# Kernel tuning notes

Hardware: AMD Instinct MI355X
Metric: run time of the kernel (lower is better)

Reference implementation:

```python
import jax, jax.numpy as jnp
import numpy as np

N_EMBD = 256
B, T = 2, 512


def setup_inputs() -> dict:
    key = jax.random.key(0)
    kx, ks, kv = jax.random.split(key, 3)
    x = jax.random.normal(kx, (B, T, N_EMBD), dtype=jnp.float32)
    # init std 0.02 per nn.init.normal_(..., std=0.02); keeps I - scaled well-conditioned
    skew_param = 0.02 * jax.random.normal(ks, (N_EMBD, N_EMBD), dtype=jnp.float32)
    vector = 0.02 * jax.random.normal(kv, (1, N_EMBD), dtype=jnp.float32)
    return {"x": x, "skew_param": skew_param, "vector": vector}


def reference(x, skew_param, vector):
    n = skew_param.shape[0]
    skew = skew_param - skew_param.T                      # (n, n), skew-symmetric
    # scaled[b,t,i,j] = x[b,t,i] * skew[i,j]  -> (B, T, n, n)
    scaled = x[..., :, None] * skew
    eye = jnp.eye(n, dtype=x.dtype)
    # Cayley transform: (I - scaled)^{-1} (I + scaled), batched over (B, T)
    q = jnp.linalg.solve(eye - scaled, eye + scaled)      # (B, T, n, n)
    # (1, n) @ (B, T, n, n) -> (B, T, n) after squeezing the row dim
    out = jnp.einsum('n,btnm->btm', vector[0], q)
    return out
```

## Files before the change

### kernel.cpp

```cpp
#include <hip/hip_runtime.h>
#include <math.h>

#define N 256
#define G 4
#define BLK 1024
#define S1 10
#define S2 8
#define SP1 11
#define VS 268
#define UTS 280
#define RIDGE 3e-5f

typedef _Float16 half8v __attribute__((ext_vector_type(8)));
typedef float float4v __attribute__((ext_vector_type(4)));

#define OFF_K     0
#define OFF_UT0   47168
#define OFF_UT1   49408
#define OFF_ZTW   51648
#define OFF_GRAM  55744
#define OFF_L     57680
#define OFF_D     59280
#define ARENA_SZ  59456

#define LD_FRAG(base, t) (*(const half8v*)((base) + (mn & 3) * UTS + 32 * (t) + 8 * mq))

#define MATVEC(basep, dst) do {                                                        \
    float4v acc0 = {0.f, 0.f, 0.f, 0.f};                                               \
    float4v acc1 = {0.f, 0.f, 0.f, 0.f};                                               \
    _Pragma("unroll")                                                                  \
    for (int t = 0; t < 4; ++t) {                                                      \
        acc0 = __builtin_amdgcn_mfma_f32_16x16x32_f16(Shi[t], LD_FRAG(basep, t), acc0, 0, 0, 0);          \
        acc1 = __builtin_amdgcn_mfma_f32_16x16x32_f16(Shi[t + 4], LD_FRAG(basep, t + 4), acc1, 0, 0, 0);  \
    }                                                                                  \
    float4v accs = acc0 + acc1;                                                        \
    if (mn < 4) *(float4v*)(zTw + wv * 64 + mn * 16 + mq * 4) = accs;                  \
    dst = zTw[wv * 64 + g * 16 + coff];                                                \
} while (0)

__global__ __launch_bounds__(BLK, 4) void cayley_v12(const float* __restrict__ x_all,
                                                     const float* __restrict__ P,
                                                     const float* __restrict__ v_in,
                                                     float* __restrict__ out, int batch) {
    __shared__ __align__(16) char arena[ARENA_SZ];
    float* sK      = (float*)(arena + OFF_K);
    _Float16* uT0  = (_Float16*)(arena + OFF_UT0);
    _Float16* uT1  = (_Float16*)(arena + OFF_UT1);
    float* zTw     = (float*)(arena + OFF_ZTW);
    float* sGram   = (float*)(arena + OFF_GRAM);
    float* sL      = (float*)(arena + OFF_L);
    float* sD      = (float*)(arena + OFF_D);

    const int tid = threadIdx.x;
    const int lane = tid & 63, wv = tid >> 6;
    const int mn = lane & 15, mq = lane >> 4;
    const int c = tid >> 2, g = tid & 3;
    const int coff = lane >> 2;
    const int sys = blockIdx.x * G + g;
    const bool alive = sys < batch;

    half8v Shi[8];
    {
        const int r = 16 * wv + mn;
#pragma unroll
        for (int t = 0; t < 8; ++t) {
            const int k0 = 32 * t + 8 * mq;
            float4v pa = *(const float4v*)(P + r * N + k0);
            float4v pb = *(const float4v*)(P + r * N + k0 + 4);
            half8v hi;
            hi[0] = (_Float16)(pa.x - P[(k0 + 0) * N + r]);
            hi[1] = (_Float16)(pa.y - P[(k0 + 1) * N + r]);
            hi[2] = (_Float16)(pa.z - P[(k0 + 2) * N + r]);
            hi[3] = (_Float16)(pa.w - P[(k0 + 3) * N + r]);
            hi[4] = (_Float16)(pb.x - P[(k0 + 4) * N + r]);
            hi[5] = (_Float16)(pb.y - P[(k0 + 5) * N + r]);
            hi[6] = (_Float16)(pb.z - P[(k0 + 6) * N + r]);
            hi[7] = (_Float16)(pb.w - P[(k0 + 7) * N + r]);
            Shi[t] = hi;
        }
    }

    const float x_own = alive ? x_all[sys * N + c] : 0.f;
    const float v_own = v_in[c];
    float wsol = 0.f;

    for (int sw = 0; sw < 2; ++sw) {
        const int s = sw ? S2 : S1;

        float kq;
        if (sw == 0) {
            kq = alive ? v_own : 0.f;
        } else {
            uT1[g * UTS + c] = (_Float16)(x_own * wsol);
            __syncthreads();
            float zm;
            MATVEC(uT1, zm);
            kq = alive ? (v_own - wsol - zm) : 0.f;
        }
        sK[g * VS + c] = kq;
        uT0[g * UTS + c] = (_Float16)(x_own * kq);
        __syncthreads();

        for (int i = 1; i <= s; ++i) {
            float zm;
            if (i & 1) { MATVEC(uT0, zm); } else { MATVEC(uT1, zm); }
            kq = 0.5f * zm;
            sK[(i * G + g) * VS + c] = kq;
            if (i < s) {
                _Float16* dst = (i & 1) ? uT1 : uT0;
                dst[g * UTS + c] = (_Float16)(x_own * kq);
            }
            __syncthreads();
        }

        const int NP = (s + 1) * (s + 2) / 2;
        for (int pp = wv; pp < NP; pp += 16) {
            int i = 0, rem = pp;
            while (rem >= (s + 1 - i)) { rem -= (s + 1 - i); ++i; }
            const int j = i + rem;
            const int gq = lane >> 4, q = lane & 15;
            const float* ka = sK + (i * G + gq) * VS + 16 * q;
            const float* kb = sK + (j * G + gq) * VS + 16 * q;
            float p;
            {
                float4v a0 = *(const float4v*)(ka);
                float4v b0 = *(const float4v*)(kb);
                float4v a1 = *(const float4v*)(ka + 4);
                float4v b1 = *(const float4v*)(kb + 4);
                p = a0.x * b0.x;
                p = fmaf(a0.y, b0.y, p); p = fmaf(a0.z, b0.z, p); p = fmaf(a0.w, b0.w, p);
                p = fmaf(a1.x, b1.x, p); p = fmaf(a1.y, b1.y, p);
                p = fmaf(a1.z, b1.z, p); p = fmaf(a1.w, b1.w, p);
            }
            {
                float4v a0 = *(const float4v*)(ka + 8);
                float4v b0 = *(const float4v*)(kb + 8);
                float4v a1 = *(const float4v*)(ka + 12);
                float4v b1 = *(const float4v*)(kb + 12);
                p = fmaf(a0.x, b0.x, p); p = fmaf(a0.y, b0.y, p);
                p = fmaf(a0.z, b0.z, p); p = fmaf(a0.w, b0.w, p);
                p = fmaf(a1.x, b1.x, p); p = fmaf(a1.y, b1.y, p);
                p = fmaf(a1.z, b1.z, p); p = fmaf(a1.w, b1.w, p);
            }
            p += __shfl_xor(p, 1); p += __shfl_xor(p, 2);
            p += __shfl_xor(p, 4); p += __shfl_xor(p, 8);
            if (q == 0) {
                sGram[(i * SP1 + j) * G + gq] = p;
                if (i != j) sGram[(j * SP1 + i) * G + gq] = p;
            }
        }
        __syncthreads();

        if (wv < 4) {
            const int gq = wv;
            const int rr = lane;
#define GG(i, j) sGram[((i) * SP1 + (j)) * G + gq]
            float invn_r = 0.f;
            if (rr < s) {
                const float Brr = GG(rr, rr) + 4.f * GG(rr, rr + 1)
                                + 4.f * GG(rr + 1, rr + 1);
                invn_r = (Brr > 1e-30f) ? (1.f / sqrtf(Brr)) : 0.f;
            }
            for (int k = 0; k < s; ++k) {
                const float invn_k = __shfl(invn_r, k);
                float a = 0.f;
                if (rr >= k && rr < s) {
                    if (rr == k) {
                        a = 1.f + RIDGE;
                    } else {
                        const float Brk = GG(rr, k) + 2.f * GG(rr, k + 1)
                                        + 2.f * GG(rr + 1, k) + 4.f * GG(rr + 1, k + 1);
                        a = Brk * invn_r * invn_k;
                    }
                    for (int m = 0; m < k; ++m)
                        a = fmaf(-sL[(rr * S1 + m) * G + gq],
                                 sL[(k * S1 + m) * G + gq], a);
                }
                float dk = __shfl(a, k);
                dk = fmaxf(dk, 0.5f * RIDGE);
                const float invd = 1.f / sqrtf(dk);
                if (rr >= k && rr < s) sL[(rr * S1 + k) * G + gq] = a * invd;
            }
            float trr = 0.f, acc = 0.f;
            const float rhs = (rr < s)
                ? (GG(rr, 0) + 2.f * GG(rr + 1, 0)) * invn_r : 0.f;
#undef GG
            for (int k = 0; k < s; ++k) {
                const float Lkk = sL[(k * S1 + k) * G + gq];
                float tk = (Lkk > 1e-20f) ? (rhs - acc) / Lkk : 0.f;
                tk = __shfl(tk, k);
                if (rr == k) trr = tk;
                if (rr > k && rr < s)
                    acc = fmaf(sL[(rr * S1 + k) * G + gq], tk, acc);
            }
            float crr = 0.f;
            acc = 0.f;
            for (int k = s - 1; k >= 0; --k) {
                const float Lkk = sL[(k * S1 + k) * G + gq];
                float ck = (Lkk > 1e-20f) ? (trr - acc) / Lkk : 0.f;
                ck = __shfl(ck, k);
                if (rr == k) crr = ck;
                if (rr < k) acc = fmaf(sL[(k * S1 + rr) * G + gq], ck, acc);
            }
            if (rr < s) sD[rr * G + gq] = crr * invn_r;
        }
        __syncthreads();

        for (int i = 0; i < s; ++i)
            wsol = fmaf(sD[i * G + g], sK[(i * G + g) * VS + c], wsol);
        __syncthreads();
    }

    if (alive) out[sys * N + c] = 2.f * wsol - v_own;
}

extern "C" void kernel_launch(void* const* d_in, const int* in_sizes, int n_in,
                              void* d_out, int out_size, void* d_ws, size_t ws_size,
                              hipStream_t stream) {
    const float* x = (const float*)d_in[0];
    const float* P = (const float*)d_in[1];
    const float* v = (const float*)d_in[2];
    float* out = (float*)d_out;
    const int batch = in_sizes[0] / N;

    const int nblk = (batch + G - 1) / G;
    hipLaunchKernelGGL(cayley_v12, dim3(nblk), dim3(BLK), 0, stream, x, P, v, out, batch);
}
```

Baseline: 98.72 us.

## Halve systems per block and give each wave two row tiles of the skew matrix

Measured after the change: 155.4 us. 1.57x slower.

```diff
diff --git a/kernel.cpp b/kernel.cpp
--- a/kernel.cpp
+++ b/kernel.cpp
@@ -2,8 +2,8 @@
 #include <math.h>
 
 #define N 256
-#define G 4
-#define BLK 1024
+#define G 2
+#define BLK 512
 #define S1 10
 #define S2 8
 #define SP1 11
@@ -15,30 +15,37 @@
 typedef float float4v __attribute__((ext_vector_type(4)));
 
 #define OFF_K     0
-#define OFF_UT0   47168
-#define OFF_UT1   49408
-#define OFF_ZTW   51648
-#define OFF_GRAM  55744
-#define OFF_L     57680
-#define OFF_D     59280
-#define ARENA_SZ  59456
-
-#define LD_FRAG(base, t) (*(const half8v*)((base) + (mn & 3) * UTS + 32 * (t) + 8 * mq))
-
-#define MATVEC(basep, dst) do {                                                        \
-    float4v acc0 = {0.f, 0.f, 0.f, 0.f};                                               \
-    float4v acc1 = {0.f, 0.f, 0.f, 0.f};                                               \
-    _Pragma("unroll")                                                                  \
-    for (int t = 0; t < 4; ++t) {                                                      \
-        acc0 = __builtin_amdgcn_mfma_f32_16x16x32_f16(Shi[t], LD_FRAG(basep, t), acc0, 0, 0, 0);          \
-        acc1 = __builtin_amdgcn_mfma_f32_16x16x32_f16(Shi[t + 4], LD_FRAG(basep, t + 4), acc1, 0, 0, 0);  \
-    }                                                                                  \
-    float4v accs = acc0 + acc1;                                                        \
-    if (mn < 4) *(float4v*)(zTw + wv * 64 + mn * 16 + mq * 4) = accs;                  \
-    dst = zTw[wv * 64 + g * 16 + coff];                                                \
+#define OFF_UT0   23584
+#define OFF_UT1   24704
+#define OFF_ZTW   25824
+#define OFF_GRAM  29920
+#define OFF_L     30896
+#define OFF_D     31696
+#define ARENA_SZ  31776
+
+#define LD_FRAG(base, t) (*(const half8v*)((base) + (mn & 1) * UTS + 32 * (t) + 8 * mq))
+
+#define MATVEC(basep, dst) do {                                                            \
+    float4v a00 = {0.f,0.f,0.f,0.f}, a01 = {0.f,0.f,0.f,0.f};                              \
+    float4v a10 = {0.f,0.f,0.f,0.f}, a11 = {0.f,0.f,0.f,0.f};                              \
+    _Pragma("unroll")                                                                      \
+    for (int t = 0; t < 4; ++t) {                                                          \
+        half8v b0 = LD_FRAG(basep, t);                                                     \
+        half8v b1 = LD_FRAG(basep, t + 4);                                                 \
+        a00 = __builtin_amdgcn_mfma_f32_16x16x32_f16(Shi[t],      b0, a00, 0, 0, 0);       \
+        a10 = __builtin_amdgcn_mfma_f32_16x16x32_f16(Shi[8 + t],  b0, a10, 0, 0, 0);       \
+        a01 = __builtin_amdgcn_mfma_f32_16x16x32_f16(Shi[4 + t],  b1, a01, 0, 0, 0);       \
+        a11 = __builtin_amdgcn_mfma_f32_16x16x32_f16(Shi[12 + t], b1, a11, 0, 0, 0);       \
+    }                                                                                      \
+    float4v s0v = a00 + a01, s1v = a10 + a11;                                              \
+    if (mn < 2) {                                                                          \
+        *(float4v*)(zTw + wv * 128 + mn * 16 + mq * 4) = s0v;                              \
+        *(float4v*)(zTw + wv * 128 + 64 + mn * 16 + mq * 4) = s1v;                         \
+    }                                                                                      \
+    dst = zTw[wv * 128 + (lane >> 5) * 64 + g * 16 + ((lane >> 1) & 15)];                  \
 } while (0)
 
-__global__ __launch_bounds__(BLK, 4) void cayley_v12(const float* __restrict__ x_all,
+__global__ __launch_bounds__(BLK, 4) void cayley_v13(const float* __restrict__ x_all,
                                                      const float* __restrict__ P,
                                                      const float* __restrict__ v_in,
                                                      float* __restrict__ out, int batch) {
@@ -54,14 +61,14 @@
     const int tid = threadIdx.x;
     const int lane = tid & 63, wv = tid >> 6;
     const int mn = lane & 15, mq = lane >> 4;
-    const int c = tid >> 2, g = tid & 3;
-    const int coff = lane >> 2;
+    const int c = tid >> 1, g = tid & 1;
     const int sys = blockIdx.x * G + g;
     const bool alive = sys < batch;
 
-    half8v Shi[8];
-    {
-        const int r = 16 * wv + mn;
+    half8v Shi[16];
+#pragma unroll
+    for (int p = 0; p < 2; ++p) {
+        const int r = 32 * wv + 16 * p + mn;
 #pragma unroll
         for (int t = 0; t < 8; ++t) {
             const int k0 = 32 * t + 8 * mq;
@@ -76,7 +83,7 @@
             hi[5] = (_Float16)(pb.y - P[(k0 + 5) * N + r]);
             hi[6] = (_Float16)(pb.z - P[(k0 + 6) * N + r]);
             hi[7] = (_Float16)(pb.w - P[(k0 + 7) * N + r]);
-            Shi[t] = hi;
+            Shi[p * 8 + t] = hi;
         }
     }
 
@@ -114,44 +121,48 @@
         }
 
         const int NP = (s + 1) * (s + 2) / 2;
-        for (int pp = wv; pp < NP; pp += 16) {
-            int i = 0, rem = pp;
-            while (rem >= (s + 1 - i)) { rem -= (s + 1 - i); ++i; }
-            const int j = i + rem;
-            const int gq = lane >> 4, q = lane & 15;
-            const float* ka = sK + (i * G + gq) * VS + 16 * q;
-            const float* kb = sK + (j * G + gq) * VS + 16 * q;
-            float p;
-            {
-                float4v a0 = *(const float4v*)(ka);
-                float4v b0 = *(const float4v*)(kb);
-                float4v a1 = *(const float4v*)(ka + 4);
-                float4v b1 = *(const float4v*)(kb + 4);
-                p = a0.x * b0.x;
-                p = fmaf(a0.y, b0.y, p); p = fmaf(a0.z, b0.z, p); p = fmaf(a0.w, b0.w, p);
-                p = fmaf(a1.x, b1.x, p); p = fmaf(a1.y, b1.y, p);
-                p = fmaf(a1.z, b1.z, p); p = fmaf(a1.w, b1.w, p);
-            }
-            {
-                float4v a0 = *(const float4v*)(ka + 8);
-                float4v b0 = *(const float4v*)(kb + 8);
-                float4v a1 = *(const float4v*)(ka + 12);
-                float4v b1 = *(const float4v*)(kb + 12);
-                p = fmaf(a0.x, b0.x, p); p = fmaf(a0.y, b0.y, p);
-                p = fmaf(a0.z, b0.z, p); p = fmaf(a0.w, b0.w, p);
-                p = fmaf(a1.x, b1.x, p); p = fmaf(a1.y, b1.y, p);
-                p = fmaf(a1.z, b1.z, p); p = fmaf(a1.w, b1.w, p);
-            }
-            p += __shfl_xor(p, 1); p += __shfl_xor(p, 2);
-            p += __shfl_xor(p, 4); p += __shfl_xor(p, 8);
-            if (q == 0) {
-                sGram[(i * SP1 + j) * G + gq] = p;
-                if (i != j) sGram[(j * SP1 + i) * G + gq] = p;
-            }
-        }
-        __syncthreads();
-
-        if (wv < 4) {
+        {
+            const int hf = lane >> 5;
+            const int q16 = lane & 15;
+            const int gq = (lane >> 4) & 1;
+            for (int pp = wv * 2 + hf; pp < NP; pp += 16) {
+                int i = 0, rem = pp;
+                while (rem >= (s + 1 - i)) { rem -= (s + 1 - i); ++i; }
+                const int j = i + rem;
+                const float* ka = sK + (i * G + gq) * VS + 16 * q16;
+                const float* kb = sK + (j * G + gq) * VS + 16 * q16;
+                float p;
+                {
+                    float4v a0 = *(const float4v*)(ka);
+                    float4v b0 = *(const float4v*)(kb);
+                    float4v a1 = *(const float4v*)(ka + 4);
+                    float4v b1 = *(const float4v*)(kb + 4);
+                    p = a0.x * b0.x;
+                    p = fmaf(a0.y, b0.y, p); p = fmaf(a0.z, b0.z, p); p = fmaf(a0.w, b0.w, p);
+                    p = fmaf(a1.x, b1.x, p); p = fmaf(a1.y, b1.y, p);
+                    p = fmaf(a1.z, b1.z, p); p = fmaf(a1.w, b1.w, p);
+                }
+                {
+                    float4v a0 = *(const float4v*)(ka + 8);
+                    float4v b0 = *(const float4v*)(kb + 8);
+                    float4v a1 = *(const float4v*)(ka + 12);
+                    float4v b1 = *(const float4v*)(kb + 12);
+                    p = fmaf(a0.x, b0.x, p); p = fmaf(a0.y, b0.y, p);
+                    p = fmaf(a0.z, b0.z, p); p = fmaf(a0.w, b0.w, p);
+                    p = fmaf(a1.x, b1.x, p); p = fmaf(a1.y, b1.y, p);
+                    p = fmaf(a1.z, b1.z, p); p = fmaf(a1.w, b1.w, p);
+                }
+                p += __shfl_xor(p, 1); p += __shfl_xor(p, 2);
+                p += __shfl_xor(p, 4); p += __shfl_xor(p, 8);
+                if (q16 == 0) {
+                    sGram[(i * SP1 + j) * G + gq] = p;
+                    if (i != j) sGram[(j * SP1 + i) * G + gq] = p;
+                }
+            }
+        }
+        __syncthreads();
+
+        if (wv < G) {
             const int gq = wv;
             const int rr = lane;
 #define GG(i, j) sGram[((i) * SP1 + (j)) * G + gq]
@@ -224,5 +235,5 @@
     const int batch = in_sizes[0] / N;
 
     const int nblk = (batch + G - 1) / G;
-    hipLaunchKernelGGL(cayley_v12, dim3(nblk), dim3(BLK), 0, stream, x, P, v, out, batch);
+    hipLaunchKernelGGL(cayley_v13, dim3(nblk), dim3(BLK), 0, stream, x, P, v, out, batch);
 }
```

## Keep matvec results in MFMA accumulator layout, dropping the LDS transpose buffer

Applied to the files above, without the earlier changes.

Result: slower. 104.5 us (+5.8%).

```diff
diff --git a/kernel.cpp b/kernel.cpp
--- a/kernel.cpp
+++ b/kernel.cpp
@@ -12,33 +12,39 @@
 #define RIDGE 3e-5f
 
 typedef _Float16 half8v __attribute__((ext_vector_type(8)));
+typedef _Float16 half4v __attribute__((ext_vector_type(4)));
 typedef float float4v __attribute__((ext_vector_type(4)));
 
 #define OFF_K     0
 #define OFF_UT0   47168
 #define OFF_UT1   49408
-#define OFF_ZTW   51648
-#define OFF_GRAM  55744
-#define OFF_L     57680
-#define OFF_D     59280
-#define ARENA_SZ  59456
+#define OFF_GRAM  51648
+#define OFF_L     53584
+#define OFF_D     55184
+#define ARENA_SZ  55360
 
 #define LD_FRAG(base, t) (*(const half8v*)((base) + (mn & 3) * UTS + 32 * (t) + 8 * mq))
 
-#define MATVEC(basep, dst) do {                                                        \
-    float4v acc0 = {0.f, 0.f, 0.f, 0.f};                                               \
-    float4v acc1 = {0.f, 0.f, 0.f, 0.f};                                               \
-    _Pragma("unroll")                                                                  \
-    for (int t = 0; t < 4; ++t) {                                                      \
-        acc0 = __builtin_amdgcn_mfma_f32_16x16x32_f16(Shi[t], LD_FRAG(basep, t), acc0, 0, 0, 0);          \
-        acc1 = __builtin_amdgcn_mfma_f32_16x16x32_f16(Shi[t + 4], LD_FRAG(basep, t + 4), acc1, 0, 0, 0);  \
-    }                                                                                  \
-    float4v accs = acc0 + acc1;                                                        \
-    if (mn < 4) *(float4v*)(zTw + wv * 64 + mn * 16 + mq * 4) = accs;                  \
-    dst = zTw[wv * 64 + g * 16 + coff];                                                \
+#define MATVEC(basep, dst4) do {                                                            \
+    float4v a0 = {0.f,0.f,0.f,0.f}, a1 = {0.f,0.f,0.f,0.f};                                 \
+    float4v a2 = {0.f,0.f,0.f,0.f}, a3 = {0.f,0.f,0.f,0.f};                                 \
+    a0 = __builtin_amdgcn_mfma_f32_16x16x32_f16(Shi[0], LD_FRAG(basep, 0), a0, 0, 0, 0);    \
+    a1 = __builtin_amdgcn_mfma_f32_16x16x32_f16(Shi[1], LD_FRAG(basep, 1), a1, 0, 0, 0);    \
+    a2 = __builtin_amdgcn_mfma_f32_16x16x32_f16(Shi[2], LD_FRAG(basep, 2), a2, 0, 0, 0);    \
+    a3 = __builtin_amdgcn_mfma_f32_16x16x32_f16(Shi[3], LD_FRAG(basep, 3), a3, 0, 0, 0);    \
+    a0 = __builtin_amdgcn_mfma_f32_16x16x32_f16(Shi[4], LD_FRAG(basep, 4), a0, 0, 0, 0);    \
+    a1 = __builtin_amdgcn_mfma_f32_16x16x32_f16(Shi[5], LD_FRAG(basep, 5), a1, 0, 0, 0);    \
+    a2 = __builtin_amdgcn_mfma_f32_16x16x32_f16(Shi[6], LD_FRAG(basep, 6), a2, 0, 0, 0);    \
+    a3 = __builtin_amdgcn_mfma_f32_16x16x32_f16(Shi[7], LD_FRAG(basep, 7), a3, 0, 0, 0);    \
+    dst4 = (a0 + a1) + (a2 + a3);                                                           \
 } while (0)
 
-__global__ __launch_bounds__(BLK, 4) void cayley_v12(const float* __restrict__ x_all,
+#define H4(xv, kv, h) do {                                                                  \
+    (h)[0] = (_Float16)((xv).x * (kv).x); (h)[1] = (_Float16)((xv).y * (kv).y);             \
+    (h)[2] = (_Float16)((xv).z * (kv).z); (h)[3] = (_Float16)((xv).w * (kv).w);             \
+} while (0)
+
+__global__ __launch_bounds__(BLK, 4) void cayley_v15(const float* __restrict__ x_all,
                                                      const float* __restrict__ P,
                                                      const float* __restrict__ v_in,
                                                      float* __restrict__ out, int batch) {
@@ -46,7 +52,6 @@
     float* sK      = (float*)(arena + OFF_K);
     _Float16* uT0  = (_Float16*)(arena + OFF_UT0);
     _Float16* uT1  = (_Float16*)(arena + OFF_UT1);
-    float* zTw     = (float*)(arena + OFF_ZTW);
     float* sGram   = (float*)(arena + OFF_GRAM);
     float* sL      = (float*)(arena + OFF_L);
     float* sD      = (float*)(arena + OFF_D);
@@ -54,10 +59,10 @@
     const int tid = threadIdx.x;
     const int lane = tid & 63, wv = tid >> 6;
     const int mn = lane & 15, mq = lane >> 4;
-    const int c = tid >> 2, g = tid & 3;
-    const int coff = lane >> 2;
-    const int sys = blockIdx.x * G + g;
-    const bool alive = sys < batch;
+    const int crow = 16 * wv + 4 * mq;
+    const bool cw = (mn < 4);
+    const int sysm = blockIdx.x * G + mn;
+    const bool alivem = cw && (sysm < batch);
 
     half8v Shi[8];
     {
@@ -80,35 +85,42 @@
         }
     }
 
-    const float x_own = alive ? x_all[sys * N + c] : 0.f;
-    const float v_own = v_in[c];
-    float wsol = 0.f;
+    const float4v v_c4 = *(const float4v*)(v_in + crow);
+    float4v x_c4 = {0.f, 0.f, 0.f, 0.f};
+    if (alivem) x_c4 = *(const float4v*)(x_all + sysm * N + crow);
+    float4v w_c4 = {0.f, 0.f, 0.f, 0.f};
 
     for (int sw = 0; sw < 2; ++sw) {
         const int s = sw ? S2 : S1;
 
-        float kq;
+        float4v kq4;
         if (sw == 0) {
-            kq = alive ? v_own : 0.f;
+            kq4 = v_c4;
         } else {
-            uT1[g * UTS + c] = (_Float16)(x_own * wsol);
+            if (cw) { half4v h; H4(x_c4, w_c4, h); *(half4v*)(uT1 + mn * UTS + crow) = h; }
             __syncthreads();
-            float zm;
-            MATVEC(uT1, zm);
-            kq = alive ? (v_own - wsol - zm) : 0.f;
-        }
-        sK[g * VS + c] = kq;
-        uT0[g * UTS + c] = (_Float16)(x_own * kq);
+            float4v zm4;
+            MATVEC(uT1, zm4);
+            kq4 = v_c4 - w_c4 - zm4;
+        }
+        if (cw) {
+            *(float4v*)(sK + mn * VS + crow) = kq4;
+            half4v h; H4(x_c4, kq4, h);
+            *(half4v*)(uT0 + mn * UTS + crow) = h;
+        }
         __syncthreads();
 
         for (int i = 1; i <= s; ++i) {
-            float zm;
-            if (i & 1) { MATVEC(uT0, zm); } else { MATVEC(uT1, zm); }
-            kq = 0.5f * zm;
-            sK[(i * G + g) * VS + c] = kq;
-            if (i < s) {
-                _Float16* dst = (i & 1) ? uT1 : uT0;
-                dst[g * UTS + c] = (_Float16)(x_own * kq);
+            float4v zm4;
+            if (i & 1) { MATVEC(uT0, zm4); } else { MATVEC(uT1, zm4); }
+            kq4 = 0.5f * zm4;
+            if (cw) {
+                *(float4v*)(sK + (i * G + mn) * VS + crow) = kq4;
+                if (i < s) {
+                    _Float16* dst = (i & 1) ? uT1 : uT0;
+                    half4v h; H4(x_c4, kq4, h);
+                    *(half4v*)(dst + mn * UTS + crow) = h;
+                }
             }
             __syncthreads();
         }
@@ -206,12 +218,16 @@
         }
         __syncthreads();
 
-        for (int i = 0; i < s; ++i)
-            wsol = fmaf(sD[i * G + g], sK[(i * G + g) * VS + c], wsol);
-        __syncthreads();
+        if (cw) {
+            for (int i = 0; i < s; ++i) {
+                const float ci = sD[i * G + mn];
+                const float4v k4 = *(const float4v*)(sK + (i * G + mn) * VS + crow);
+                w_c4 += ci * k4;
+            }
+        }
     }
 
-    if (alive) out[sys * N + c] = 2.f * wsol - v_own;
+    if (alivem) *(float4v*)(out + sysm * N + crow) = 2.f * w_c4 - v_c4;
 }
 
 extern "C" void kernel_launch(void* const* d_in, const int* in_sizes, int n_in,
@@ -224,5 +240,5 @@
     const int batch = in_sizes[0] / N;
 
     const int nblk = (batch + G - 1) / G;
-    hipLaunchKernelGGL(cayley_v12, dim3(nblk), dim3(BLK), 0, stream, x, P, v, out, batch);
+    hipLaunchKernelGGL(cayley_v15, dim3(nblk), dim3(BLK), 0, stream, x, P, v, out, batch);
 }
```
